# Optimization experiments

Hardware: AMD Instinct MI355X
Metric: run time of the kernel (lower is better)

The kernel has to match this reference:

```python
import jax, jax.numpy as jnp
import numpy as np

B, S, HID = 1, 4096, 1024
HQ, HKV, D = 16, 4, 64   # query heads, kv heads (GQA), dim_per_head
ROPE_BASE = 10000.0


def setup_inputs() -> dict:
    key = jax.random.key(0)
    ks = jax.random.split(key, 5)
    s = 0.02
    return {
        "x": jax.random.normal(ks[0], (B, S, HID), jnp.float32),
        "Wq": jax.random.normal(ks[1], (HID, HQ * D), jnp.float32) * s,
        "Wk": jax.random.normal(ks[2], (HID, HKV * D), jnp.float32) * s,
        "Wv": jax.random.normal(ks[3], (HID, HKV * D), jnp.float32) * s,
        "Wo": jax.random.normal(ks[4], (HQ * D, HID), jnp.float32) * s,
    }


def _rope(t, cos, sin):
    # non-interleaved (half-split) rotary; t: [B,S,H,D], cos/sin: [S, D//2]
    t1, t2 = jnp.split(t, 2, axis=-1)
    c = cos[None, :, None, :]
    sn = sin[None, :, None, :]
    return jnp.concatenate([t1 * c - t2 * sn, t2 * c + t1 * sn], axis=-1)


def reference(x, Wq, Wk, Wv, Wo):
    # QKV projections (self-attention: key=value=query=x), reshape to [B,S,H,D]
    q = (x @ Wq).reshape(B, S, HQ, D)
    k = (x @ Wk).reshape(B, S, HKV, D)
    v = (x @ Wv).reshape(B, S, HKV, D)

    # rotary position embedding over full head dim
    inv_freq = 1.0 / (ROPE_BASE ** (jnp.arange(0, D, 2, dtype=jnp.float32) / D))
    ang = jnp.arange(S, dtype=jnp.float32)[:, None] * inv_freq[None, :]  # [S, D//2]
    cos, sin = jnp.cos(ang), jnp.sin(ang)
    q = _rope(q, cos, sin)
    k = _rope(k, cos, sin)

    # GQA: expand kv heads to match query heads
    g = HQ // HKV
    k = jnp.repeat(k, g, axis=2)
    v = jnp.repeat(v, g, axis=2)

    scale = D ** -0.5  # attn_scaling ** -0.5 with attn_scaling = dim_per_head
    scores = jnp.einsum('bqhd,bkhd->bhqk', q, k) * scale  # [B,HQ,S,S]
    causal = jnp.tril(jnp.ones((S, S), dtype=bool))
    scores = jnp.where(causal[None, None], scores, jnp.finfo(scores.dtype).min)
    attn = jax.nn.softmax(scores, axis=-1)

    ctx = jnp.einsum('bhqk,bkhd->bqhd', attn, v).reshape(B, S, HQ * D)
    return ctx @ Wo
```

## Files before the change

kernel.cpp:

```cpp
#include <hip/hip_runtime.h>
#include <hip/hip_bf16.h>
#include <math.h>

typedef __attribute__((ext_vector_type(8))) short short8;
typedef __attribute__((ext_vector_type(4))) float f32x4;

#define S_   4096
#define HQ_  16
#define HKV_ 4
#define D_   64

static __device__ __forceinline__ unsigned short f2b(float f) {
    __hip_bfloat16 h = __float2bfloat16(f);
    return *reinterpret_cast<unsigned short*>(&h);
}
static __device__ __forceinline__ float b2f(unsigned short u) {
    union { unsigned int u; float f; } c;
    c.u = ((unsigned int)u) << 16;
    return c.f;
}

typedef __attribute__((address_space(1))) const unsigned int gas_u32;
typedef __attribute__((address_space(3))) unsigned int las_u32;
static __device__ __forceinline__ void gload16(const void* g, void* l) {
    __builtin_amdgcn_global_load_lds((gas_u32*)g, (las_u32*)l, 16, 0, 0);
}


__global__ __launch_bounds__(256) void k_prep(const float* __restrict__ Wq,
                                              const float* __restrict__ Wk,
                                              const float* __restrict__ Wv,
                                              const float* __restrict__ Wo,
                                              const float* __restrict__ x,
                                              unsigned short* __restrict__ WT,
                                              unsigned short* __restrict__ WoT,
                                              unsigned short* __restrict__ xb,
                                              float* __restrict__ cs) {
    const int z = blockIdx.z;
    const int t = threadIdx.x;
    if (z == 4) {
        int flat = blockIdx.y * 32 + blockIdx.x;
#pragma unroll
        for (int ii = 0; ii < 4; ++ii) {
            int i = flat * 1024 + ii * 256 + t;
            float4 v = ((const float4*)x)[i];
            ushort4 o;
            o.x = f2b(v.x); o.y = f2b(v.y); o.z = f2b(v.z); o.w = f2b(v.w);
            ((ushort4*)xb)[i] = o;
        }
        return;
    }
    if (z == 5) {
        int flat = blockIdx.y * 32 + blockIdx.x;
        if (flat >= 512) return;
        int i = flat * 256 + t;
        int s = i >> 5, jj = i & 31;
        float invf = exp2f(-(float)jj * (13.287712379549449f / 32.0f));
        float ang = (float)s * invf;
        ((float2*)cs)[i] = make_float2(cosf(ang), sinf(ang));
        return;
    }
    const float* tin; unsigned short* tout; int N, gx;
    if (z == 0)      { tin = Wq; tout = WT;                 N = 1024; gx = 32; }
    else if (z == 1) { tin = Wk; tout = WT + 1024 * 1024;   N = 256;  gx = 8;  }
    else if (z == 2) { tin = Wv; tout = WT + 1280 * 1024;   N = 256;  gx = 8;  }
    else             { tin = Wo; tout = WoT;                N = 1024; gx = 32; }
    if ((int)blockIdx.x >= gx) return;
    __shared__ float tile[32][33];
    int tx = t & 31, ty = t >> 5;
    int n0 = blockIdx.x * 32, k0 = blockIdx.y * 32;
#pragma unroll
    for (int r = 0; r < 32; r += 8)
        tile[ty + r][tx] = tin[(size_t)(k0 + ty + r) * N + n0 + tx];
    __syncthreads();
#pragma unroll
    for (int r = 0; r < 32; r += 8)
        tout[(size_t)(n0 + ty + r) * 1024 + k0 + tx] = f2b(tile[tx][ty + r]);
}


__global__ __launch_bounds__(256, 3)
void k_gemm_qkv(const unsigned short* __restrict__ A,
                const unsigned short* __restrict__ BT,
                const float* __restrict__ cs,
                unsigned short* __restrict__ Qr,
                unsigned short* __restrict__ Kr,
                unsigned short* __restrict__ Vp) {
    __shared__ unsigned short As[128 * 128];
    __shared__ unsigned short Bs[64 * 128];
    const int t = threadIdx.x;
    const int ntile = blockIdx.x;
    const int n0 = ntile * 64;
    const int m0 = blockIdx.y * 128;
    const int w = t >> 6, lane = t & 63, lr = lane & 15, lg = lane >> 4;
    const int srr = w * 4 + (lane >> 4);
    const int sby = (lane & 15) * 16;
    const int K = 1024;

    f32x4 acc[2][4];
#pragma unroll
    for (int m = 0; m < 2; ++m)
#pragma unroll
        for (int n = 0; n < 4; ++n) acc[m][n] = (f32x4){0.f, 0.f, 0.f, 0.f};

    for (int k0 = 0; k0 < K; k0 += 128) {
#pragma unroll
        for (int c = 0; c < 8; ++c) {
            int r = c * 16 + srr;
            gload16((const char*)&A[(size_t)(m0 + r) * K + k0] + (sby ^ ((r & 7) << 4)),
                    (char*)As + c * 4096 + w * 1024);
        }
#pragma unroll
        for (int c = 0; c < 4; ++c) {
            int r = c * 16 + srr;
            gload16((const char*)&BT[(size_t)(n0 + r) * K + k0] + (sby ^ ((r & 7) << 4)),
                    (char*)Bs + c * 4096 + w * 1024);
        }
        __syncthreads();
#pragma unroll
        for (int kk = 0; kk < 4; ++kk) {
            short8 af[2], bf[4];
#pragma unroll
            for (int m = 0; m < 2; ++m) {
                int arow = w * 32 + m * 16 + lr;
                af[m] = *(const short8*)((const char*)As + arow * 256 +
                                         ((kk * 64 + lg * 16) ^ ((arow & 7) << 4)));
            }
#pragma unroll
            for (int n = 0; n < 4; ++n) {
                int brow = n * 16 + lr;
                bf[n] = *(const short8*)((const char*)Bs + brow * 256 +
                                         ((kk * 64 + lg * 16) ^ ((brow & 7) << 4)));
            }
#pragma unroll
            for (int m = 0; m < 2; ++m)
#pragma unroll
                for (int n = 0; n < 4; ++n)
                    acc[m][n] = __builtin_amdgcn_mfma_f32_16x16x32_bf16(af[m], bf[n], acc[m][n], 0, 0, 0);
        }
        __syncthreads();
    }

    if (ntile < 20) {
        const float QS = (ntile < 16) ? 0.125f * 1.44269504088896340736f : 1.0f;
        unsigned short* dst = (ntile < 16) ? (Qr + (size_t)ntile * (S_ * D_))
                                           : (Kr + (size_t)(ntile - 16) * (S_ * D_));
#pragma unroll
        for (int m = 0; m < 2; ++m)
#pragma unroll
            for (int rr = 0; rr < 4; ++rr) {
                int s = m0 + w * 32 + m * 16 + lg * 4 + rr;
                const float2* csr = (const float2*)cs + s * 32;
                float2 c0 = csr[lr];
                float2 c1 = csr[16 + lr];
                float t1 = acc[m][0][rr], t2 = acc[m][2][rr];
                dst[(size_t)s * 64 + lr]      = f2b((t1 * c0.x - t2 * c0.y) * QS);
                dst[(size_t)s * 64 + 32 + lr] = f2b((t2 * c0.x + t1 * c0.y) * QS);
                t1 = acc[m][1][rr]; t2 = acc[m][3][rr];
                dst[(size_t)s * 64 + 16 + lr] = f2b((t1 * c1.x - t2 * c1.y) * QS);
                dst[(size_t)s * 64 + 48 + lr] = f2b((t2 * c1.x + t1 * c1.y) * QS);
            }
    } else {
        int h2 = ntile - 20;
        unsigned short* dst = Vp + (size_t)h2 * (D_ * S_);
#pragma unroll
        for (int m = 0; m < 2; ++m)
#pragma unroll
            for (int n = 0; n < 4; ++n) {
                int d = n * 16 + lr;
                int pos = m0 + (w >> 1) * 64 + (w & 1) * 32 + lg * 8 + m * 4;
                ushort4 o;
                o.x = f2b(acc[m][n][0]); o.y = f2b(acc[m][n][1]);
                o.z = f2b(acc[m][n][2]); o.w = f2b(acc[m][n][3]);
                *(ushort4*)&dst[(size_t)d * S_ + pos] = o;
            }
    }
}


__global__ __launch_bounds__(256, 3)
void k_gemm_o(const unsigned short* __restrict__ A,
              const unsigned short* __restrict__ BT,
              float* __restrict__ out) {
    __shared__ unsigned short As[128 * 128];
    __shared__ unsigned short Bs[64 * 128];
    const int t = threadIdx.x;
    const int n0 = blockIdx.x * 64;
    const int m0 = blockIdx.y * 128;
    const int w = t >> 6, lane = t & 63, lr = lane & 15, lg = lane >> 4;
    const int srr = w * 4 + (lane >> 4);
    const int sby = (lane & 15) * 16;
    const int K = 1024;

    f32x4 acc[2][4];
#pragma unroll
    for (int m = 0; m < 2; ++m)
#pragma unroll
        for (int n = 0; n < 4; ++n) acc[m][n] = (f32x4){0.f, 0.f, 0.f, 0.f};

    for (int k0 = 0; k0 < K; k0 += 128) {
#pragma unroll
        for (int c = 0; c < 8; ++c) {
            int r = c * 16 + srr;
            gload16((const char*)&A[(size_t)(m0 + r) * K + k0] + (sby ^ ((r & 7) << 4)),
                    (char*)As + c * 4096 + w * 1024);
        }
#pragma unroll
        for (int c = 0; c < 4; ++c) {
            int r = c * 16 + srr;
            gload16((const char*)&BT[(size_t)(n0 + r) * K + k0] + (sby ^ ((r & 7) << 4)),
                    (char*)Bs + c * 4096 + w * 1024);
        }
        __syncthreads();
#pragma unroll
        for (int kk = 0; kk < 4; ++kk) {
            short8 af[2], bf[4];
#pragma unroll
            for (int m = 0; m < 2; ++m) {
                int arow = w * 32 + m * 16 + lr;
                af[m] = *(const short8*)((const char*)As + arow * 256 +
                                         ((kk * 64 + lg * 16) ^ ((arow & 7) << 4)));
            }
#pragma unroll
            for (int n = 0; n < 4; ++n) {
                int brow = n * 16 + lr;
                bf[n] = *(const short8*)((const char*)Bs + brow * 256 +
                                         ((kk * 64 + lg * 16) ^ ((brow & 7) << 4)));
            }
#pragma unroll
            for (int m = 0; m < 2; ++m)
#pragma unroll
                for (int n = 0; n < 4; ++n)
                    acc[m][n] = __builtin_amdgcn_mfma_f32_16x16x32_bf16(af[m], bf[n], acc[m][n], 0, 0, 0);
        }
        __syncthreads();
    }
#pragma unroll
    for (int m = 0; m < 2; ++m)
#pragma unroll
        for (int n = 0; n < 4; ++n)
#pragma unroll
            for (int rr = 0; rr < 4; ++rr) {
                int row = m0 + w * 32 + m * 16 + lg * 4 + rr;
                int col = n0 + n * 16 + lr;
                out[(size_t)row * 1024 + col] = acc[m][n][rr];
            }
}


__global__ __launch_bounds__(256, 4)
void k_attn(const unsigned short* __restrict__ Qr,
            const unsigned short* __restrict__ Kr,
            const unsigned short* __restrict__ Vp,
            unsigned short* __restrict__ Pacc,
            float* __restrict__ Psv) {
    __shared__ unsigned short Ks[2][64 * 64];
    __shared__ unsigned short Vs[2][64 * 64];

    const int t = threadIdx.x;
    const int p = blockIdx.x;
    const int h = blockIdx.y;
    const int j = blockIdx.z;
    const int kvh = h >> 2;
    const int w = t >> 6, lane = t & 63, lr = lane & 15, lg = lane >> 4;

    const unsigned short* Qh = Qr + (size_t)h * (S_ * D_);
    const unsigned short* Kh = Kr + (size_t)kvh * (S_ * D_);
    const unsigned short* Vh = Vp + (size_t)kvh * (D_ * S_);

    const int xw = (lr & 7) << 4;
    const int sr = lane >> 3, sch = (lane & 7) * 16;
    const int r0a = w * 16, r0b = w * 16 + 8;

#pragma unroll 1
    for (int half = 0; half < 2; ++half) {
        const int qb = half ? p : (63 - p);
        const int tend = qb + 1;
        const int qi = qb * 64 + w * 16 + lr;

        const char* kp[2];
        const char* vp[2];
        {
            int ra = r0a + sr, rb = r0b + sr;
            kp[0] = (const char*)(Kh + (size_t)(j * 64 + ra) * 64) + (sch ^ ((ra & 7) << 4));
            kp[1] = (const char*)(Kh + (size_t)(j * 64 + rb) * 64) + (sch ^ ((rb & 7) << 4));
            vp[0] = (const char*)(Vh + (size_t)ra * S_ + j * 64) + (sch ^ ((ra & 7) << 4));
            vp[1] = (const char*)(Vh + (size_t)rb * S_ + j * 64) + (sch ^ ((rb & 7) << 4));
        }
        auto stage = [&](int buf) {
            gload16(kp[0], (char*)&Ks[buf][0] + r0a * 128);
            gload16(kp[1], (char*)&Ks[buf][0] + r0b * 128);
            gload16(vp[0], (char*)&Vs[buf][0] + r0a * 128);
            gload16(vp[1], (char*)&Vs[buf][0] + r0b * 128);
            kp[0] += 16384; kp[1] += 16384;
            vp[0] += 256;   vp[1] += 256;
        };

        short8 aq[2];
        {
            int qrow = qb * 64 + w * 16 + lr;
            aq[0] = *(const short8*)&Qh[(size_t)qrow * 64 + lg * 8];
            aq[1] = *(const short8*)&Qh[(size_t)qrow * 64 + 32 + lg * 8];
        }
        float svl = 0.f;
        f32x4 acc_o[4];
#pragma unroll
        for (int i = 0; i < 4; ++i) acc_o[i] = (f32x4){0.f, 0.f, 0.f, 0.f};

        int cur = 0;
        stage(0);
        __syncthreads();

        for (int kb = j; kb < tend; kb += 2) {
            if (kb + 2 < tend) stage(cur ^ 1);

            f32x4 s[4];
#pragma unroll
            for (int i = 0; i < 4; ++i) s[i] = (f32x4){0.f, 0.f, 0.f, 0.f};
            const char* KsB = (const char*)&Ks[cur][0];
            __builtin_amdgcn_s_setprio(1);
#pragma unroll
            for (int kk = 0; kk < 2; ++kk)
#pragma unroll
                for (int nt = 0; nt < 4; ++nt) {
                    short8 kf = *(const short8*)(KsB + (nt * 16 + lr) * 128 + ((kk * 64 + lg * 16) ^ xw));
                    s[nt] = __builtin_amdgcn_mfma_f32_16x16x32_bf16(kf, aq[kk], s[nt], 0, 0, 0);
                }
            __builtin_amdgcn_s_setprio(0);

            if (kb == qb) {
                int kbase = kb * 64 + lg * 4;
#pragma unroll
                for (int nt = 0; nt < 4; ++nt)
#pragma unroll
                    for (int rr = 0; rr < 4; ++rr)
                        if (kbase + nt * 16 + rr > qi) s[nt][rr] = -INFINITY;
            }

            unsigned int wd[8];
#pragma unroll
            for (int nt = 0; nt < 4; ++nt) {
                float p0 = exp2f(s[nt][0]), p1 = exp2f(s[nt][1]);
                float p2 = exp2f(s[nt][2]), p3 = exp2f(s[nt][3]);
                svl += (p0 + p1) + (p2 + p3);
                asm("v_cvt_pk_bf16_f32 %0, %1, %2" : "=v"(wd[nt * 2])     : "v"(p0), "v"(p1));
                asm("v_cvt_pk_bf16_f32 %0, %1, %2" : "=v"(wd[nt * 2 + 1]) : "v"(p2), "v"(p3));
            }

            const char* VsB = (const char*)&Vs[cur][0];
            __builtin_amdgcn_s_setprio(1);
#pragma unroll
            for (int kk = 0; kk < 2; ++kk) {
                union { unsigned int u[4]; short8 s8; } pa;
                pa.u[0] = wd[4 * kk + 0]; pa.u[1] = wd[4 * kk + 1];
                pa.u[2] = wd[4 * kk + 2]; pa.u[3] = wd[4 * kk + 3];
#pragma unroll
                for (int nt = 0; nt < 4; ++nt) {
                    short8 vb = *(const short8*)(VsB + (nt * 16 + lr) * 128 + ((kk * 64 + lg * 16) ^ xw));
                    acc_o[nt] = __builtin_amdgcn_mfma_f32_16x16x32_bf16(pa.s8, vb, acc_o[nt], 0, 0, 0);
                }
            }
            __builtin_amdgcn_s_setprio(0);

            __syncthreads();
            cur ^= 1;
        }

        svl += __shfl_xor(svl, 16);
        svl += __shfl_xor(svl, 32);
        const int u = ((j * 64 + qb) * 16 + h);
        if (lg == 0) Psv[u * 64 + w * 16 + lr] = svl;
        unsigned short* Pb = Pacc + (size_t)u * 4096;
#pragma unroll
        for (int nt = 0; nt < 4; ++nt) {
            int rr = w * 16 + lg * 4;
            int col = nt * 16 + lr;
            Pb[(rr + 0) * 64 + col] = f2b(acc_o[nt][0]);
            Pb[(rr + 1) * 64 + col] = f2b(acc_o[nt][1]);
            Pb[(rr + 2) * 64 + col] = f2b(acc_o[nt][2]);
            Pb[(rr + 3) * 64 + col] = f2b(acc_o[nt][3]);
        }
    }
}


__global__ __launch_bounds__(256) void k_combine(const unsigned short* __restrict__ Pacc,
                                                 const float* __restrict__ Psv,
                                                 unsigned short* __restrict__ O) {
    const int qb = blockIdx.x, h = blockIdx.y;
    const int t = threadIdx.x;
    const int r = t >> 2, db = (t & 3) * 16;
    const int u0 = (qb * 16 + h);
    const int u1 = ((64 + qb) * 16 + h);
    float sa = Psv[u0 * 64 + r], sb = Psv[u1 * 64 + r];
    float inv = 1.f / (sa + sb);
    const unsigned short* A_ = Pacc + (size_t)u0 * 4096 + r * 64 + db;
    const unsigned short* B_ = Pacc + (size_t)u1 * 4096 + r * 64 + db;
    unsigned short* Op = O + (size_t)(qb * 64 + r) * 1024 + h * 64 + db;
#pragma unroll
    for (int halfv = 0; halfv < 2; ++halfv) {
        short8 va = *(const short8*)(A_ + halfv * 8);
        short8 vb = *(const short8*)(B_ + halfv * 8);
        short8 o;
#pragma unroll
        for (int i = 0; i < 8; ++i)
            o[i] = (short)f2b((b2f((unsigned short)va[i]) + b2f((unsigned short)vb[i])) * inv);
        *(short8*)(Op + halfv * 8) = o;
    }
}


extern "C" void kernel_launch(void* const* d_in, const int* in_sizes, int n_in,
                              void* d_out, int out_size, void* d_ws, size_t ws_size,
                              hipStream_t stream) {
    const float* x  = (const float*)d_in[0];
    const float* Wq = (const float*)d_in[1];
    const float* Wk = (const float*)d_in[2];
    const float* Wv = (const float*)d_in[3];
    const float* Wo = (const float*)d_in[4];
    float* out = (float*)d_out;
    char* ws = (char*)d_ws;

    unsigned short* WT  = (unsigned short*)(ws + 0);
    unsigned short* WoT = (unsigned short*)(ws + 3145728);
    unsigned short* Qr  = (unsigned short*)(ws + 5242880);
    unsigned short* Kr  = (unsigned short*)(ws + 13631488);
    unsigned short* Vp  = (unsigned short*)(ws + 15728640);
    unsigned short* O   = (unsigned short*)(ws + 17825792);
    float* cs           = (float*)(ws + 26214400);
    unsigned short* xb  = (unsigned short*)(ws + 27262976);
    unsigned short* Pacc = (unsigned short*)(ws + 27262976);
    float* Psv           = (float*)(ws + 44040192);

    k_prep<<<dim3(32, 32, 6), 256, 0, stream>>>(Wq, Wk, Wv, Wo, x, WT, WoT, xb, cs);
    k_gemm_qkv<<<dim3(24, 32), 256, 0, stream>>>(xb, WT, cs, Qr, Kr, Vp);
    k_attn<<<dim3(32, 16, 2), 256, 0, stream>>>(Qr, Kr, Vp, Pacc, Psv);
    k_combine<<<dim3(64, 16), 256, 0, stream>>>(Pacc, Psv, O);
    k_gemm_o<<<dim3(16, 32), 256, 0, stream>>>(O, WoT, out);
}
```

Measured before the change: 116.6 us.

## Double-buffer LDS staging in QKV and output projection GEMMs

Both projection GEMMs now split K into 64-wide steps with two LDS buffers, prefetching the next tile with async global-to-LDS loads while MFMAs consume the current one. This replaces the old single 128-wide stage that had to load and sync before any compute. Wave priority is raised during the MFMA section. Total LDS per block stays the same, but there are twice as many loop iterations and barriers. Correctness depends on async loads completing before the end-of-iteration barrier.

```diff
diff --git a/kernel.cpp b/kernel.cpp
--- a/kernel.cpp
+++ b/kernel.cpp
@@ -86,15 +86,14 @@
                 unsigned short* __restrict__ Qr,
                 unsigned short* __restrict__ Kr,
                 unsigned short* __restrict__ Vp) {
-    __shared__ unsigned short As[128 * 128];
-    __shared__ unsigned short Bs[64 * 128];
+    __shared__ unsigned short As[2][128 * 64];
+    __shared__ unsigned short Bs[2][64 * 64];
     const int t = threadIdx.x;
     const int ntile = blockIdx.x;
     const int n0 = ntile * 64;
     const int m0 = blockIdx.y * 128;
     const int w = t >> 6, lane = t & 63, lr = lane & 15, lg = lane >> 4;
-    const int srr = w * 4 + (lane >> 4);
-    const int sby = (lane & 15) * 16;
+    const int sr = lane >> 3, sch = (lane & 7) * 16;
     const int K = 1024;
 
     f32x4 acc[2][4];
@@ -103,33 +102,45 @@
 #pragma unroll
         for (int n = 0; n < 4; ++n) acc[m][n] = (f32x4){0.f, 0.f, 0.f, 0.f};
 
-    for (int k0 = 0; k0 < K; k0 += 128) {
-#pragma unroll
-        for (int c = 0; c < 8; ++c) {
-            int r = c * 16 + srr;
-            gload16((const char*)&A[(size_t)(m0 + r) * K + k0] + (sby ^ ((r & 7) << 4)),
-                    (char*)As + c * 4096 + w * 1024);
-        }
+    auto stage = [&](int buf, int k0) {
 #pragma unroll
         for (int c = 0; c < 4; ++c) {
-            int r = c * 16 + srr;
-            gload16((const char*)&BT[(size_t)(n0 + r) * K + k0] + (sby ^ ((r & 7) << 4)),
-                    (char*)Bs + c * 4096 + w * 1024);
-        }
-        __syncthreads();
-#pragma unroll
-        for (int kk = 0; kk < 4; ++kk) {
+            int r0 = w * 32 + c * 8;
+            int r = r0 + sr;
+            gload16((const char*)&A[(size_t)(m0 + r) * K + k0] + (sch ^ ((r & 7) << 4)),
+                    (char*)&As[buf][0] + r0 * 128);
+        }
+#pragma unroll
+        for (int c = 0; c < 2; ++c) {
+            int r0 = w * 16 + c * 8;
+            int r = r0 + sr;
+            gload16((const char*)&BT[(size_t)(n0 + r) * K + k0] + (sch ^ ((r & 7) << 4)),
+                    (char*)&Bs[buf][0] + r0 * 128);
+        }
+    };
+
+    int cur = 0;
+    stage(0, 0);
+    __syncthreads();
+
+    for (int k0 = 0; k0 < K; k0 += 64) {
+        if (k0 + 64 < K) stage(cur ^ 1, k0 + 64);
+        const char* AsB = (const char*)&As[cur][0];
+        const char* BsB = (const char*)&Bs[cur][0];
+        __builtin_amdgcn_s_setprio(1);
+#pragma unroll
+        for (int kk = 0; kk < 2; ++kk) {
             short8 af[2], bf[4];
 #pragma unroll
             for (int m = 0; m < 2; ++m) {
                 int arow = w * 32 + m * 16 + lr;
-                af[m] = *(const short8*)((const char*)As + arow * 256 +
+                af[m] = *(const short8*)(AsB + arow * 128 +
                                          ((kk * 64 + lg * 16) ^ ((arow & 7) << 4)));
             }
 #pragma unroll
             for (int n = 0; n < 4; ++n) {
                 int brow = n * 16 + lr;
-                bf[n] = *(const short8*)((const char*)Bs + brow * 256 +
+                bf[n] = *(const short8*)(BsB + brow * 128 +
                                          ((kk * 64 + lg * 16) ^ ((brow & 7) << 4)));
             }
 #pragma unroll
@@ -138,7 +149,9 @@
                 for (int n = 0; n < 4; ++n)
                     acc[m][n] = __builtin_amdgcn_mfma_f32_16x16x32_bf16(af[m], bf[n], acc[m][n], 0, 0, 0);
         }
+        __builtin_amdgcn_s_setprio(0);
         __syncthreads();
+        cur ^= 1;
     }
 
     if (ntile < 20) {
@@ -182,14 +195,13 @@
 void k_gemm_o(const unsigned short* __restrict__ A,
               const unsigned short* __restrict__ BT,
               float* __restrict__ out) {
-    __shared__ unsigned short As[128 * 128];
-    __shared__ unsigned short Bs[64 * 128];
+    __shared__ unsigned short As[2][128 * 64];
+    __shared__ unsigned short Bs[2][64 * 64];
     const int t = threadIdx.x;
     const int n0 = blockIdx.x * 64;
     const int m0 = blockIdx.y * 128;
     const int w = t >> 6, lane = t & 63, lr = lane & 15, lg = lane >> 4;
-    const int srr = w * 4 + (lane >> 4);
-    const int sby = (lane & 15) * 16;
+    const int sr = lane >> 3, sch = (lane & 7) * 16;
     const int K = 1024;
 
     f32x4 acc[2][4];
@@ -198,33 +210,45 @@
 #pragma unroll
         for (int n = 0; n < 4; ++n) acc[m][n] = (f32x4){0.f, 0.f, 0.f, 0.f};
 
-    for (int k0 = 0; k0 < K; k0 += 128) {
-#pragma unroll
-        for (int c = 0; c < 8; ++c) {
-            int r = c * 16 + srr;
-            gload16((const char*)&A[(size_t)(m0 + r) * K + k0] + (sby ^ ((r & 7) << 4)),
-                    (char*)As + c * 4096 + w * 1024);
-        }
+    auto stage = [&](int buf, int k0) {
 #pragma unroll
         for (int c = 0; c < 4; ++c) {
-            int r = c * 16 + srr;
-            gload16((const char*)&BT[(size_t)(n0 + r) * K + k0] + (sby ^ ((r & 7) << 4)),
-                    (char*)Bs + c * 4096 + w * 1024);
-        }
-        __syncthreads();
-#pragma unroll
-        for (int kk = 0; kk < 4; ++kk) {
+            int r0 = w * 32 + c * 8;
+            int r = r0 + sr;
+            gload16((const char*)&A[(size_t)(m0 + r) * K + k0] + (sch ^ ((r & 7) << 4)),
+                    (char*)&As[buf][0] + r0 * 128);
+        }
+#pragma unroll
+        for (int c = 0; c < 2; ++c) {
+            int r0 = w * 16 + c * 8;
+            int r = r0 + sr;
+            gload16((const char*)&BT[(size_t)(n0 + r) * K + k0] + (sch ^ ((r & 7) << 4)),
+                    (char*)&Bs[buf][0] + r0 * 128);
+        }
+    };
+
+    int cur = 0;
+    stage(0, 0);
+    __syncthreads();
+
+    for (int k0 = 0; k0 < K; k0 += 64) {
+        if (k0 + 64 < K) stage(cur ^ 1, k0 + 64);
+        const char* AsB = (const char*)&As[cur][0];
+        const char* BsB = (const char*)&Bs[cur][0];
+        __builtin_amdgcn_s_setprio(1);
+#pragma unroll
+        for (int kk = 0; kk < 2; ++kk) {
             short8 af[2], bf[4];
 #pragma unroll
             for (int m = 0; m < 2; ++m) {
                 int arow = w * 32 + m * 16 + lr;
-                af[m] = *(const short8*)((const char*)As + arow * 256 +
+                af[m] = *(const short8*)(AsB + arow * 128 +
                                          ((kk * 64 + lg * 16) ^ ((arow & 7) << 4)));
             }
 #pragma unroll
             for (int n = 0; n < 4; ++n) {
                 int brow = n * 16 + lr;
-                bf[n] = *(const short8*)((const char*)Bs + brow * 256 +
+                bf[n] = *(const short8*)(BsB + brow * 128 +
                                          ((kk * 64 + lg * 16) ^ ((brow & 7) << 4)));
             }
 #pragma unroll
@@ -233,7 +257,9 @@
                 for (int n = 0; n < 4; ++n)
                     acc[m][n] = __builtin_amdgcn_mfma_f32_16x16x32_bf16(af[m], bf[n], acc[m][n], 0, 0, 0);
         }
+        __builtin_amdgcn_s_setprio(0);
         __syncthreads();
+        cur ^= 1;
     }
 #pragma unroll
     for (int m = 0; m < 2; ++m)
```

Result: no change. 114.6 us (median of 2 runs) (-1.7%).
